# Performance work log

Measured on AMD Instinct MI355X. Metric: run time of the kernel, lower is better.

The kernel has to match this reference:

```python
import jax, jax.numpy as jnp
import numpy as np

N_NODES = 50000
N_EDGES = 1600000
D_IN = 128
D_HID = 128


def setup_inputs() -> dict:
    key = jax.random.key(0)
    ks = jax.random.split(key, 6)
    edge_index = jax.random.randint(ks[0], (2, N_EDGES), 0, N_NODES, dtype=jnp.int32)
    emb = jax.random.normal(ks[1], (N_NODES, D_IN), dtype=jnp.float32) * 0.1
    W1 = jax.random.normal(ks[2], (D_IN, D_HID), dtype=jnp.float32) * (1.0 / np.sqrt(D_IN))
    b1 = jnp.zeros((D_HID,), dtype=jnp.float32)
    W2 = jax.random.normal(ks[3], (D_HID, D_HID), dtype=jnp.float32) * (1.0 / np.sqrt(D_HID))
    b2 = jnp.zeros((D_HID,), dtype=jnp.float32)
    head_w = jax.random.normal(ks[4], (D_HID, 1), dtype=jnp.float32) * (1.0 / np.sqrt(D_HID))
    head_b = jnp.zeros((1,), dtype=jnp.float32)
    return {"edge_index": edge_index, "emb": emb, "W1": W1, "b1": b1,
            "W2": W2, "b2": b2, "head_w": head_w, "head_b": head_b}


def _gcn_norm(edge_index, num_nodes):
    # PyG GCNConv default: add self-loops, sym-normalize D^-1/2 (A+I) D^-1/2.
    loops = jnp.arange(num_nodes, dtype=edge_index.dtype)
    src = jnp.concatenate([edge_index[0], loops])  # [E+N]
    dst = jnp.concatenate([edge_index[1], loops])  # [E+N]
    deg = jax.ops.segment_sum(jnp.ones_like(dst, dtype=jnp.float32), dst,
                              num_segments=num_nodes)  # [N], >=1 via self-loops
    dis = jax.lax.rsqrt(deg)
    norm = dis[src] * dis[dst]  # [E+N]
    return src, dst, norm


def _gcn_conv(x, W, b, src, dst, norm, num_nodes):
    h = x @ W                                  # [N, D] dense transform first
    msg = h[src] * norm[:, None]               # [E+N, D] gather + scale
    out = jax.ops.segment_sum(msg, dst, num_segments=num_nodes)  # scatter-add
    return out + b


def reference(edge_index, emb, W1, b1, W2, b2, head_w, head_b):
    src, dst, norm = _gcn_norm(edge_index, N_NODES)
    x = jax.nn.relu(_gcn_conv(emb, W1, b1, src, dst, norm, N_NODES))
    x = jax.nn.relu(_gcn_conv(x, W2, b2, src, dst, norm, N_NODES))
    scores = jax.nn.sigmoid(x @ head_w + head_b)[:, 0]  # [N]
    return scores
```

## Files before the change

kernel.cpp:

```cpp
#include <hip/hip_runtime.h>
#include <hip/hip_fp16.h>
#include <math.h>

#define D 128
#define D4 32
#define AP 136
#define AP8 144
#define NBUCK 512
#define NT 512
#define EPB 4096
#define BCAP2 4096

typedef _Float16 f16x8 __attribute__((ext_vector_type(8)));
typedef float f32x4 __attribute__((ext_vector_type(4)));
typedef float f32x2 __attribute__((ext_vector_type(2)));


__global__ void prep_all_kernel(const float* __restrict__ W1, _Float16* __restrict__ Wt1,
                                const float* __restrict__ W2, _Float16* __restrict__ Wt2,
                                int* __restrict__ bcnt) {
    int t = threadIdx.x;
    if (blockIdx.x == 0) { bcnt[t] = 0; bcnt[256 + t] = 0; }
    int half = blockIdx.x & 63;
    const float* W = (blockIdx.x < 64) ? W1 : W2;
    _Float16* Wt   = (blockIdx.x < 64) ? Wt1 : Wt2;
    int i = half * 256 + t;
    int k = i >> 7, c = i & 127;
    Wt[c * 128 + k] = (_Float16)W[i];
}


__global__ __launch_bounds__(NT) void bucket_pass1(const int* __restrict__ src,
                                                   const int* __restrict__ dst,
                                                   int* __restrict__ bcnt,
                                                   unsigned* __restrict__ buckets,
                                                   int E, unsigned magicM) {
    __shared__ unsigned stage[EPB];
    __shared__ int lcnt[NBUCK], loff[NBUCK], gbase[NBUCK];

    int t = threadIdx.x;
    int base = blockIdx.x * EPB;
    int nblk = min(EPB, E - base);
    lcnt[t] = 0;
    __syncthreads();

    for (int i = t; i < nblk; i += NT) {
        unsigned d = (unsigned)dst[base + i];
        int b = (int)(((unsigned long long)d * magicM) >> 24);
        atomicAdd(&lcnt[b], 1);
    }
    __syncthreads();

    int v = lcnt[t];
    loff[t] = v;
    __syncthreads();
    for (int off = 1; off < NT; off <<= 1) {
        int x = (t >= off) ? loff[t - off] : 0;
        __syncthreads();
        loff[t] += x;
        __syncthreads();
    }
    int incl = loff[t];
    __syncthreads();
    loff[t] = incl - v;
    gbase[t] = atomicAdd(&bcnt[t], v);
    lcnt[t] = 0;
    __syncthreads();

    for (int i = t; i < nblk; i += NT) {
        unsigned s = (unsigned)src[base + i];
        unsigned d = (unsigned)dst[base + i];
        unsigned pk = (s << 16) | d;
        int b = (int)(((unsigned long long)d * magicM) >> 24);
        int p = atomicAdd(&lcnt[b], 1);
        stage[loff[b] + p] = pk;
    }
    __syncthreads();

    for (int i = t; i < nblk; i += NT) {
        unsigned pk = stage[i];
        int b = (int)(((unsigned long long)(pk & 0xffffu) * magicM) >> 24);
        int pos = gbase[b] + (i - loff[b]);
        if (pos < BCAP2) buckets[(size_t)b * BCAP2 + pos] = pk;
    }
}

__global__ __launch_bounds__(NT) void csr_pass2(const unsigned* __restrict__ buckets,
                                                const int* __restrict__ bcnt,
                                                int* __restrict__ row_ptr,
                                                float* __restrict__ dis,
                                                unsigned short* __restrict__ col,
                                                int N, int npb, int E) {
    __shared__ int cnt[NT], sc[NT], excl[NT];
    __shared__ unsigned short estage[BCAP2];

    int b = blockIdx.x;
    int t = threadIdx.x;

    int bv = min(bcnt[t], BCAP2);
    sc[t] = bv;
    __syncthreads();
    for (int off = 1; off < NT; off <<= 1) {
        int x = (t >= off) ? sc[t - off] : 0;
        __syncthreads();
        sc[t] += x;
        __syncthreads();
    }
    int base = sc[b] - min(bcnt[b], BCAP2);
    if (b == 0 && t == 0) row_ptr[N] = E;
    __syncthreads();

    int lo = b * npb;
    int nn = min(npb, N - lo);
    int n = min(bcnt[b], BCAP2);
    const unsigned* bk = buckets + (size_t)b * BCAP2;

    cnt[t] = 0;
    __syncthreads();
    for (int i = t; i < n; i += NT) {
        int dl = (int)(bk[i] & 0xffffu) - lo;
        atomicAdd(&cnt[dl], 1);
    }
    __syncthreads();
    int v = cnt[t];
    sc[t] = v;
    __syncthreads();
    for (int off = 1; off < NT; off <<= 1) {
        int x = (t >= off) ? sc[t - off] : 0;
        __syncthreads();
        sc[t] += x;
        __syncthreads();
    }
    excl[t] = sc[t] - v;
    if (t < nn) {
        row_ptr[lo + t] = base + excl[t];
        dis[lo + t] = rsqrtf((float)v + 1.0f);
    }
    cnt[t] = 0;
    __syncthreads();
    for (int i = t; i < n; i += NT) {
        unsigned pk = bk[i];
        int dl = (int)(pk & 0xffffu) - lo;
        int p = atomicAdd(&cnt[dl], 1);
        estage[excl[dl] + p] = (unsigned short)(pk >> 16);
    }
    __syncthreads();
    for (int i = t; i < n; i += NT) col[base + i] = estage[i];
}


#define GEMM_CORE                                                            \
    const uint4* Wt16 = (const uint4*)Wt;                                    \
    for (int i = t; i < 128 * 16; i += 256) {                                \
        int r = i >> 4, ch = i & 15;                                         \
        *(uint4*)&Ws[r * AP + ch * 8] = Wt16[i];                             \
    }                                                                        \
    __syncthreads();                                                         \
    int wave = t >> 6;                                                       \
    int lane = t & 63;                                                       \
    int m16 = lane & 15;                                                     \
    int quad = lane >> 4;                                                    \
    f32x4 acc[8];                                                            \
    for (int n = 0; n < 8; n++) acc[n] = (f32x4){0.f, 0.f, 0.f, 0.f};        \
    _Pragma("unroll")                                                        \
    for (int kc = 0; kc < 4; kc++) {                                         \
        f16x8 a = *(const f16x8*)&As[(wave * 16 + m16) * AP + kc * 32 + quad * 8]; \
        _Pragma("unroll")                                                    \
        for (int n = 0; n < 8; n++) {                                        \
            f16x8 bfrag = *(const f16x8*)&Ws[(n * 16 + m16) * AP + kc * 32 + quad * 8]; \
            acc[n] = __builtin_amdgcn_mfma_f32_16x16x32_f16(a, bfrag, acc[n], 0, 0, 0); \
        }                                                                    \
    }                                                                        \
    __syncthreads();                                                         \
    unsigned char* Cs8 = (unsigned char*)As;                                 \
    float dv[4];                                                             \
    _Pragma("unroll")                                                        \
    for (int r = 0; r < 4; r++) {                                            \
        int grow = row0 + wave * 16 + quad * 4 + r;                          \
        dv[r] = (grow < N) ? dis[grow] : 0.f;                                \
    }                                                                        \
    _Pragma("unroll")                                                        \
    for (int n = 0; n < 8; n++)                                              \
        _Pragma("unroll")                                                    \
        for (int r = 0; r < 4; r++) {                                        \
            float val = acc[n][r] * dv[r];                                   \
            int wq = __builtin_amdgcn_cvt_pk_fp8_f32(val, val, 0, false);    \
            Cs8[(wave * 16 + quad * 4 + r) * AP8 + n * 16 + m16] = (unsigned char)(wq & 0xff); \
        }                                                                    \
    __syncthreads();                                                         \
    uint4* C16 = (uint4*)C8;                                                 \
    for (int i = lane; i < 128; i += 64) {                                   \
        int r = i >> 3, ch = i & 7;                                          \
        int grow = row0 + wave * 16 + r;                                     \
        if (grow < N)                                                        \
            C16[(size_t)grow * 8 + ch] = *(const uint4*)&Cs8[(wave * 16 + r) * AP8 + ch * 16]; \
    }

__global__ __launch_bounds__(256) void gemm_f32a_fp8c(const float* __restrict__ A,
                                                      const _Float16* __restrict__ Wt,
                                                      const float* __restrict__ dis,
                                                      unsigned int* __restrict__ C8, int N) {
    __shared__ _Float16 As[64 * AP];
    __shared__ _Float16 Ws[128 * AP];
    int t = threadIdx.x;
    int row0 = blockIdx.x * 64;
    const float4* A4 = (const float4*)A;
    for (int i = t; i < 64 * 16; i += 256) {
        int r = i >> 4, ch = i & 15;
        uint4 v = make_uint4(0, 0, 0, 0);
        if (row0 + r < N) {
            float4 a0 = A4[(size_t)(row0 + r) * 32 + ch * 2];
            float4 a1 = A4[(size_t)(row0 + r) * 32 + ch * 2 + 1];
            __half2 h0 = __floats2half2_rn(a0.x, a0.y);
            __half2 h1 = __floats2half2_rn(a0.z, a0.w);
            __half2 h2 = __floats2half2_rn(a1.x, a1.y);
            __half2 h3 = __floats2half2_rn(a1.z, a1.w);
            v.x = *(unsigned*)&h0; v.y = *(unsigned*)&h1;
            v.z = *(unsigned*)&h2; v.w = *(unsigned*)&h3;
        }
        *(uint4*)&As[r * AP + ch * 8] = v;
    }
    GEMM_CORE
}

__global__ __launch_bounds__(256) void gemm_f16a_fp8c(const _Float16* __restrict__ A,
                                                      const _Float16* __restrict__ Wt,
                                                      const float* __restrict__ dis,
                                                      unsigned int* __restrict__ C8, int N) {
    __shared__ _Float16 As[64 * AP];
    __shared__ _Float16 Ws[128 * AP];
    int t = threadIdx.x;
    int row0 = blockIdx.x * 64;
    const uint4* A16 = (const uint4*)A;
    for (int i = t; i < 64 * 16; i += 256) {
        int r = i >> 4, ch = i & 15;
        uint4 v = make_uint4(0, 0, 0, 0);
        if (row0 + r < N) v = A16[(size_t)(row0 + r) * 16 + ch];
        *(uint4*)&As[r * AP + ch * 8] = v;
    }
    GEMM_CORE
}


__device__ __forceinline__ void acc8(float4& a, unsigned int u) {
    f32x2 lo = __builtin_amdgcn_cvt_pk_f32_fp8((int)u, false);
    f32x2 hi = __builtin_amdgcn_cvt_pk_f32_fp8((int)u, true);
    a.x += lo[0]; a.y += lo[1]; a.z += hi[0]; a.w += hi[1];
}

#define AGG8_BODY                                                               \
    float4 acc = make_float4(0.f, 0.f, 0.f, 0.f);                               \
    acc8(acc, t8[(size_t)node * D4 + lane]);        \
    int e0 = row_ptr[node], e1 = row_ptr[node + 1];                             \
    int deg = e1 - e0;                                                          \
    for (int base = 0; base < deg; base += 32) {                                \
        int cnt = min(32, deg - base);                                          \
        int myc = (base + lane < deg) ? (int)col[e0 + base + lane] : 0;         \
        int j = 0;                                                              \
        for (; j + 8 <= cnt; j += 8) {                                          \
            int s0 = __shfl(myc, j + 0, 32); int s1 = __shfl(myc, j + 1, 32);   \
            int s2 = __shfl(myc, j + 2, 32); int s3 = __shfl(myc, j + 3, 32);   \
            int s4 = __shfl(myc, j + 4, 32); int s5 = __shfl(myc, j + 5, 32);   \
            int s6 = __shfl(myc, j + 6, 32); int s7 = __shfl(myc, j + 7, 32);   \
            unsigned int u0 = t8[(size_t)s0 * D4 + lane];                       \
            unsigned int u1 = t8[(size_t)s1 * D4 + lane];                       \
            unsigned int u2 = t8[(size_t)s2 * D4 + lane];                       \
            unsigned int u3 = t8[(size_t)s3 * D4 + lane];                       \
            unsigned int u4 = t8[(size_t)s4 * D4 + lane];                       \
            unsigned int u5 = t8[(size_t)s5 * D4 + lane];                       \
            unsigned int u6 = t8[(size_t)s6 * D4 + lane];                       \
            unsigned int u7 = t8[(size_t)s7 * D4 + lane];                       \
            acc8(acc, u0); acc8(acc, u1); acc8(acc, u2); acc8(acc, u3);         \
            acc8(acc, u4); acc8(acc, u5); acc8(acc, u6); acc8(acc, u7);         \
        }                                                                       \
        for (; j < cnt; j++) {                                                  \
            int s = __shfl(myc, j, 32);                                         \
            acc8(acc, t8[(size_t)s * D4 + lane]);                               \
        }                                                                       \
    }                                                                           \
    float di = dis[node];                                                       \
    float4 bb = ((const float4*)bias)[lane];                                    \
    float4 o;                                                                   \
    o.x = fmaxf(fmaf(di, acc.x, bb.x), 0.f);                                    \
    o.y = fmaxf(fmaf(di, acc.y, bb.y), 0.f);                                    \
    o.z = fmaxf(fmaf(di, acc.z, bb.z), 0.f);                                    \
    o.w = fmaxf(fmaf(di, acc.w, bb.w), 0.f);

__global__ void agg_fp8_kernel(const unsigned int* __restrict__ t8, const float* __restrict__ bias,
                               const int* __restrict__ row_ptr, const unsigned short* __restrict__ col,
                               const float* __restrict__ dis, _Float16* __restrict__ xout, int N) {
    int t = threadIdx.x;
    int node = blockIdx.x * 8 + (t >> 5);
    int lane = t & 31;
    if (node >= N) return;
    AGG8_BODY
    __half2 q0 = __floats2half2_rn(o.x, o.y);
    __half2 q1 = __floats2half2_rn(o.z, o.w);
    uint2 u;
    u.x = *(unsigned int*)&q0;
    u.y = *(unsigned int*)&q1;
    ((uint2*)xout)[(size_t)node * D4 + lane] = u;
}

__global__ void agg_head_fp8_kernel(const unsigned int* __restrict__ t8, const float* __restrict__ bias,
                                    const int* __restrict__ row_ptr, const unsigned short* __restrict__ col,
                                    const float* __restrict__ dis,
                                    const float* __restrict__ head_w, const float* __restrict__ head_b,
                                    float* __restrict__ out, int N) {
    int t = threadIdx.x;
    int node = blockIdx.x * 8 + (t >> 5);
    int lane = t & 31;
    if (node >= N) return;
    AGG8_BODY
    float4 wv = ((const float4*)head_w)[lane];
    float s = o.x * wv.x + o.y * wv.y + o.z * wv.z + o.w * wv.w;
    for (int m = 1; m < 32; m <<= 1) s += __shfl_xor(s, m, 64);
    if (lane == 0) {
        float v = s + head_b[0];
        out[node] = 1.0f / (1.0f + expf(-v));
    }
}


extern "C" void kernel_launch(void* const* d_in, const int* in_sizes, int n_in,
                              void* d_out, int out_size, void* d_ws, size_t ws_size,
                              hipStream_t stream) {
    const int*   edge   = (const int*)d_in[0];
    const float* emb    = (const float*)d_in[1];
    const float* W1     = (const float*)d_in[2];
    const float* b1     = (const float*)d_in[3];
    const float* W2     = (const float*)d_in[4];
    const float* b2     = (const float*)d_in[5];
    const float* head_w = (const float*)d_in[6];
    const float* head_b = (const float*)d_in[7];
    float* out = (float*)d_out;

    int E = in_sizes[0] / 2;
    int N = in_sizes[1] / D;
    const int* srcp = edge;
    const int* dstp = edge + E;

    char* w = (char*)d_ws;
    auto alloc = [&](size_t bytes) -> char* {
        char* p = w;
        w += (bytes + 15) & ~(size_t)15;
        return p;
    };
    unsigned int*   t8      = (unsigned int*)alloc((size_t)N * D);
    _Float16*       x1h     = (_Float16*)alloc((size_t)N * D * 2);
    unsigned*       buckets = (unsigned*)alloc((size_t)NBUCK * BCAP2 * 4);
    _Float16*       Wt1     = (_Float16*)alloc((size_t)D * D * 2);
    _Float16*       Wt2     = (_Float16*)alloc((size_t)D * D * 2);
    unsigned short* col     = (unsigned short*)alloc((size_t)E * 2);
    int*            bcnt    = (int*)alloc(NBUCK * 4);
    int*            row_ptr = (int*)alloc((size_t)(N + 1) * 4);
    float*          dis     = (float*)alloc((size_t)N * 4);

    int npb = (N + NBUCK - 1) / NBUCK;
    unsigned magicM = (16777216u + (unsigned)npb - 1) / (unsigned)npb;
    int gP1 = (E + EPB - 1) / EPB;
    int gG = (N + 63) / 64;
    int gA = (N + 7) / 8;

    prep_all_kernel<<<128, 256, 0, stream>>>(W1, Wt1, W2, Wt2, bcnt);
    bucket_pass1<<<gP1, NT, 0, stream>>>(srcp, dstp, bcnt, buckets, E, magicM);
    csr_pass2<<<NBUCK, NT, 0, stream>>>(buckets, bcnt, row_ptr, dis, col, N, npb, E);

    gemm_f32a_fp8c<<<gG, 256, 0, stream>>>(emb, Wt1, dis, t8, N);
    agg_fp8_kernel<<<gA, 256, 0, stream>>>(t8, b1, row_ptr, col, dis, x1h, N);
    gemm_f16a_fp8c<<<gG, 256, 0, stream>>>(x1h, Wt2, dis, t8, N);
    agg_head_fp8_kernel<<<gA, 256, 0, stream>>>(t8, b2, row_ptr, col, dis,
                                                head_w, head_b, out, N);
}
```

Before: 194.9 us.

## Use wave-shuffle scans, register-cached edges, and nontemporal loads/stores

Replaces the 512-thread shared-memory Hillis-Steele scans in both CSR-build kernels with a wave-level shuffle scan plus a cross-wave sum, which needs far fewer barriers. In bucket_pass1 each thread loads its 8 edges into registers once, so src and dst are not read from global memory twice. Streaming reads in the GEMM A loads and the aggregation col reads, and the fp16 output store, are switched to nontemporal hints to reduce cache pollution. The nontemporal hints could hurt if the data is actually reused from cache, for example the fp16 activations written by the aggregation and then read by the next GEMM.

After: 203.2 us. 1.04x slower.

```diff
diff --git a/kernel.cpp b/kernel.cpp
--- a/kernel.cpp
+++ b/kernel.cpp
@@ -14,6 +14,8 @@
 typedef _Float16 f16x8 __attribute__((ext_vector_type(8)));
 typedef float f32x4 __attribute__((ext_vector_type(4)));
 typedef float f32x2 __attribute__((ext_vector_type(2)));
+typedef unsigned u32x4 __attribute__((ext_vector_type(4)));
+typedef unsigned u32x2 __attribute__((ext_vector_type(2)));
 
 
 __global__ void prep_all_kernel(const float* __restrict__ W1, _Float16* __restrict__ Wt1,
@@ -30,6 +32,24 @@
 }
 
 
+__device__ __forceinline__ int scan_incl_512(int v, int t, int* wsum) {
+    int lane = t & 63, wid = t >> 6;
+    __syncthreads();
+    int x = v;
+    #pragma unroll
+    for (int off = 1; off < 64; off <<= 1) {
+        int y = __shfl_up(x, off, 64);
+        if (lane >= off) x += y;
+    }
+    if (lane == 63) wsum[wid] = x;
+    __syncthreads();
+    int add = 0;
+    #pragma unroll
+    for (int wj = 0; wj < 8; ++wj) add += (wj < wid) ? wsum[wj] : 0;
+    return x + add;
+}
+
+
 __global__ __launch_bounds__(NT) void bucket_pass1(const int* __restrict__ src,
                                                    const int* __restrict__ dst,
                                                    int* __restrict__ bcnt,
@@ -37,51 +57,56 @@
                                                    int E, unsigned magicM) {
     __shared__ unsigned stage[EPB];
     __shared__ int lcnt[NBUCK], loff[NBUCK], gbase[NBUCK];
+    __shared__ int wsum[8];
 
     int t = threadIdx.x;
     int base = blockIdx.x * EPB;
     int nblk = min(EPB, E - base);
     lcnt[t] = 0;
-    __syncthreads();
-
-    for (int i = t; i < nblk; i += NT) {
-        unsigned d = (unsigned)dst[base + i];
-        int b = (int)(((unsigned long long)d * magicM) >> 24);
-        atomicAdd(&lcnt[b], 1);
+
+    unsigned pk[8];
+    #pragma unroll
+    for (int k = 0; k < 8; ++k) {
+        int i = t + k * NT;
+        if (i < nblk) {
+            unsigned s = (unsigned)__builtin_nontemporal_load(src + base + i);
+            unsigned d = (unsigned)__builtin_nontemporal_load(dst + base + i);
+            pk[k] = (s << 16) | d;
+        } else pk[k] = 0xffffffffu;
+    }
+    __syncthreads();
+
+    #pragma unroll
+    for (int k = 0; k < 8; ++k) {
+        if (pk[k] != 0xffffffffu) {
+            int b = (int)(((unsigned long long)(pk[k] & 0xffffu) * magicM) >> 24);
+            atomicAdd(&lcnt[b], 1);
+        }
     }
     __syncthreads();
 
     int v = lcnt[t];
-    loff[t] = v;
-    __syncthreads();
-    for (int off = 1; off < NT; off <<= 1) {
-        int x = (t >= off) ? loff[t - off] : 0;
-        __syncthreads();
-        loff[t] += x;
-        __syncthreads();
-    }
-    int incl = loff[t];
-    __syncthreads();
+    int incl = scan_incl_512(v, t, wsum);
     loff[t] = incl - v;
     gbase[t] = atomicAdd(&bcnt[t], v);
     lcnt[t] = 0;
     __syncthreads();
 
+    #pragma unroll
+    for (int k = 0; k < 8; ++k) {
+        if (pk[k] != 0xffffffffu) {
+            int b = (int)(((unsigned long long)(pk[k] & 0xffffu) * magicM) >> 24);
+            int p = atomicAdd(&lcnt[b], 1);
+            stage[loff[b] + p] = pk[k];
+        }
+    }
+    __syncthreads();
+
     for (int i = t; i < nblk; i += NT) {
-        unsigned s = (unsigned)src[base + i];
-        unsigned d = (unsigned)dst[base + i];
-        unsigned pk = (s << 16) | d;
-        int b = (int)(((unsigned long long)d * magicM) >> 24);
-        int p = atomicAdd(&lcnt[b], 1);
-        stage[loff[b] + p] = pk;
-    }
-    __syncthreads();
-
-    for (int i = t; i < nblk; i += NT) {
-        unsigned pk = stage[i];
-        int b = (int)(((unsigned long long)(pk & 0xffffu) * magicM) >> 24);
+        unsigned q = stage[i];
+        int b = (int)(((unsigned long long)(q & 0xffffu) * magicM) >> 24);
         int pos = gbase[b] + (i - loff[b]);
-        if (pos < BCAP2) buckets[(size_t)b * BCAP2 + pos] = pk;
+        if (pos < BCAP2) buckets[(size_t)b * BCAP2 + pos] = q;
     }
 }
 
@@ -92,23 +117,17 @@
                                                 unsigned short* __restrict__ col,
                                                 int N, int npb, int E) {
     __shared__ int cnt[NT], sc[NT], excl[NT];
+    __shared__ int wsum[8];
     __shared__ unsigned short estage[BCAP2];
 
     int b = blockIdx.x;
     int t = threadIdx.x;
 
     int bv = min(bcnt[t], BCAP2);
-    sc[t] = bv;
-    __syncthreads();
-    for (int off = 1; off < NT; off <<= 1) {
-        int x = (t >= off) ? sc[t - off] : 0;
-        __syncthreads();
-        sc[t] += x;
-        __syncthreads();
-    }
+    sc[t] = scan_incl_512(bv, t, wsum);
+    __syncthreads();
     int base = sc[b] - min(bcnt[b], BCAP2);
     if (b == 0 && t == 0) row_ptr[N] = E;
-    __syncthreads();
 
     int lo = b * npb;
     int nn = min(npb, N - lo);
@@ -123,15 +142,8 @@
     }
     __syncthreads();
     int v = cnt[t];
-    sc[t] = v;
-    __syncthreads();
-    for (int off = 1; off < NT; off <<= 1) {
-        int x = (t >= off) ? sc[t - off] : 0;
-        __syncthreads();
-        sc[t] += x;
-        __syncthreads();
-    }
-    excl[t] = sc[t] - v;
+    int incl = scan_incl_512(v, t, wsum);
+    excl[t] = incl - v;
     if (t < nn) {
         row_ptr[lo + t] = base + excl[t];
         dis[lo + t] = rsqrtf((float)v + 1.0f);
@@ -204,13 +216,13 @@
     __shared__ _Float16 Ws[128 * AP];
     int t = threadIdx.x;
     int row0 = blockIdx.x * 64;
-    const float4* A4 = (const float4*)A;
+    const f32x4* A4 = (const f32x4*)A;
     for (int i = t; i < 64 * 16; i += 256) {
         int r = i >> 4, ch = i & 15;
         uint4 v = make_uint4(0, 0, 0, 0);
         if (row0 + r < N) {
-            float4 a0 = A4[(size_t)(row0 + r) * 32 + ch * 2];
-            float4 a1 = A4[(size_t)(row0 + r) * 32 + ch * 2 + 1];
+            f32x4 a0 = __builtin_nontemporal_load(&A4[(size_t)(row0 + r) * 32 + ch * 2]);
+            f32x4 a1 = __builtin_nontemporal_load(&A4[(size_t)(row0 + r) * 32 + ch * 2 + 1]);
             __half2 h0 = __floats2half2_rn(a0.x, a0.y);
             __half2 h1 = __floats2half2_rn(a0.z, a0.w);
             __half2 h2 = __floats2half2_rn(a1.x, a1.y);
@@ -231,12 +243,12 @@
     __shared__ _Float16 Ws[128 * AP];
     int t = threadIdx.x;
     int row0 = blockIdx.x * 64;
-    const uint4* A16 = (const uint4*)A;
+    const u32x4* A16 = (const u32x4*)A;
     for (int i = t; i < 64 * 16; i += 256) {
         int r = i >> 4, ch = i & 15;
-        uint4 v = make_uint4(0, 0, 0, 0);
-        if (row0 + r < N) v = A16[(size_t)(row0 + r) * 16 + ch];
-        *(uint4*)&As[r * AP + ch * 8] = v;
+        u32x4 v = (u32x4){0u, 0u, 0u, 0u};
+        if (row0 + r < N) v = __builtin_nontemporal_load(&A16[(size_t)(row0 + r) * 16 + ch]);
+        *(u32x4*)&As[r * AP + ch * 8] = v;
     }
     GEMM_CORE
 }
@@ -255,7 +267,9 @@
     int deg = e1 - e0;                                                          \
     for (int base = 0; base < deg; base += 32) {                                \
         int cnt = min(32, deg - base);                                          \
-        int myc = (base + lane < deg) ? (int)col[e0 + base + lane] : 0;         \
+        int myc = (base + lane < deg)                                           \
+                    ? (int)__builtin_nontemporal_load(col + e0 + base + lane)   \
+                    : 0;                                                        \
         int j = 0;                                                              \
         for (; j + 8 <= cnt; j += 8) {                                          \
             int s0 = __shfl(myc, j + 0, 32); int s1 = __shfl(myc, j + 1, 32);   \
@@ -296,10 +310,10 @@
     AGG8_BODY
     __half2 q0 = __floats2half2_rn(o.x, o.y);
     __half2 q1 = __floats2half2_rn(o.z, o.w);
-    uint2 u;
+    u32x2 u;
     u.x = *(unsigned int*)&q0;
     u.y = *(unsigned int*)&q1;
-    ((uint2*)xout)[(size_t)node * D4 + lane] = u;
+    __builtin_nontemporal_store(u, (u32x2*)xout + (size_t)node * D4 + lane);
 }
 
 __global__ void agg_head_fp8_kernel(const unsigned int* __restrict__ t8, const float* __restrict__ bias,
```
